# Performance work log

Hardware: AMD Instinct MI355X
Metric: run time of the kernel (lower is better)

## Reference

```python
import jax, jax.numpy as jnp
import numpy as np
from jax import lax

TAU = 10.0
THR = 1.0
ALPHA = float(np.exp(-1.0 / TAU))  # leak factor exp(-dt/tau), dt=1


def conv2d(x, w, pad):
    # x: [N,C,H,W], w: [O,I,kh,kw]
    return lax.conv_general_dilated(
        x, w, window_strides=(1, 1), padding=[(pad, pad), (pad, pad)],
        dimension_numbers=('NCHW', 'OIHW', 'NCHW'))


def avgpool(x, k):
    n, c, h, w = x.shape
    return x.reshape(n, c, h // k, k, w // k, k).mean(axis=(3, 5))


def exp_leak(x):
    # x: [T, ...]; v[t] = alpha*v[t-1] + x[t]; outputs membrane each step
    def step(v, xt):
        v = ALPHA * v + xt
        return v, v
    _, y = lax.scan(step, jnp.zeros_like(x[0]), x)
    return y


def lif(x):
    # LIF with SingleSpike + MembraneSubtract reset (norm_input=False)
    def step(v, xt):
        v = ALPHA * v + xt
        s = (v >= THR).astype(v.dtype)
        return v - s * THR, s
    _, s = lax.scan(step, jnp.zeros_like(x[0]), x)
    return s


def forward(x, conv1_w, conv2_w, lin_w):
    B, T = x.shape[:2]
    h = avgpool(conv2d(x.reshape(B * T, 2, 32, 32), conv1_w, 2), 4)  # [BT,4,8,8]
    h = h.reshape(B, T, 4, 8, 8).swapaxes(0, 1)                       # [T,B,4,8,8]
    h = lif(exp_leak(h)).swapaxes(0, 1).reshape(B * T, 4, 8, 8)
    h = avgpool(conv2d(h, conv2_w, 1), 2)                             # [BT,8,4,4]
    h = h.reshape(B, T, 8, 4, 4).swapaxes(0, 1)                       # [T,B,8,4,4]
    h = lif(exp_leak(h)).swapaxes(0, 1).reshape(B, T, 8 * 4 * 4)      # [B,T,128]
    return jnp.einsum('btf,of->bto', h, lin_w)                        # [B,T,2]


def setup_inputs() -> dict:
    key = jax.random.key(0)
    k1, k2, k3, k4 = jax.random.split(key, 4)
    B, T = 128, 100
    x = jax.random.uniform(k1, (B, T, 2, 32, 32), dtype=jnp.float32)
    conv1_w = jax.random.normal(k2, (4, 2, 5, 5), dtype=jnp.float32) / np.sqrt(2 * 5 * 5)
    conv2_w = jax.random.normal(k3, (8, 4, 3, 3), dtype=jnp.float32) / np.sqrt(4 * 3 * 3)
    lin_w = jax.random.normal(k4, (2, 128), dtype=jnp.float32) / np.sqrt(128)
    return {'x': x, 'conv1_w': conv1_w, 'conv2_w': conv2_w, 'lin_w': lin_w}


def reference(x, conv1_w, conv2_w, lin_w):
    return forward(x, conv1_w, conv2_w, lin_w)
```

## Files before the change

kernel.cpp:

```cpp
#include <hip/hip_runtime.h>

#define ALPHA 0.90483741803595957f

__global__ void prep_weights(const float* __restrict__ w1, const float* __restrict__ w2,
                             float* __restrict__ w1e, float* __restrict__ w2e) {
    int idx = blockIdx.x * 256 + threadIdx.x;
    if (idx < 512) {
        int v = idx & 7, u = (idx >> 3) & 7, ch = (idx >> 6) & 1, oc = idx >> 7;
        float s = 0.f;
        for (int a = 0; a < 5; ++a) {
            int i = u - a; if (i < 0 || i > 3) continue;
            for (int b = 0; b < 5; ++b) {
                int j = v - b; if (j < 0 || j > 3) continue;
                s += w1[((oc * 2 + ch) * 5 + a) * 5 + b];
            }
        }
        w1e[idx] = s * (1.f / 16.f);
    } else if (idx < 1024) {
        int k = idx - 512;
        int v = k & 3, u = (k >> 2) & 3, ch = (k >> 4) & 3, oc = k >> 6;
        float s = 0.f;
        for (int a = 0; a < 3; ++a) {
            int i = u - a; if (i < 0 || i > 1) continue;
            for (int b = 0; b < 3; ++b) {
                int j = v - b; if (j < 0 || j > 1) continue;
                s += w2[((oc * 4 + ch) * 3 + a) * 3 + b];
            }
        }
        w2e[k] = s * 0.25f;
    }
}

__global__ __launch_bounds__(256) void conv1_pool(const float* __restrict__ x,
                                                  const float* __restrict__ w1e,
                                                  float* __restrict__ y1) {
    __shared__ __align__(16) float tile[4][2][36][40];
    __shared__ __align__(16) float wlds[512];
    int tid = threadIdx.x;

    float4* t4 = (float4*)&tile[0][0][0][0];
    #pragma unroll
    for (int k = 0; k < 12; ++k) {
        int i = tid + k * 256;
        if (i < 2880) t4[i] = make_float4(0.f, 0.f, 0.f, 0.f);
    }
    for (int j = tid; j < 512; j += 256) {
        int oc = j >> 7, ch = (j >> 6) & 1, r = (j >> 3) & 7, c = j & 7;
        wlds[((ch * 8 + r) * 4 + oc) * 8 + c] = w1e[j];
    }
    __syncthreads();

    int w = tid >> 6, lane = tid & 63;
    long gi = (long)blockIdx.x * 4 + w;
    const float* src = x + gi * 2048;
    #pragma unroll
    for (int k = 0; k < 8; ++k) {
        int e = k * 256 + lane * 4;
        float4 d = *(const float4*)(src + e);
        int ch = e >> 10, rem = e & 1023, r = rem >> 5, c = rem & 31;
        float* dst = &tile[w][ch][r + 2][c + 2];
        *(float2*)dst = make_float2(d.x, d.y);
        *(float2*)(dst + 2) = make_float2(d.z, d.w);
    }

    int p = lane >> 3, q = lane & 7;
    float acc0 = 0.f, acc1 = 0.f, acc2 = 0.f, acc3 = 0.f;
    #pragma unroll
    for (int ch = 0; ch < 2; ++ch) {
        #pragma unroll
        for (int r = 0; r < 8; ++r) {
            const float* row = &tile[w][ch][4 * p + r][4 * q];
            float4 a = *(const float4*)row;
            float4 b = *(const float4*)(row + 4);
            const float* wr = &wlds[(ch * 8 + r) * 32];
            float4 wa, wb;
            wa = *(const float4*)(wr + 0);  wb = *(const float4*)(wr + 4);
            acc0 += wa.x * a.x + wa.y * a.y + wa.z * a.z + wa.w * a.w
                  + wb.x * b.x + wb.y * b.y + wb.z * b.z + wb.w * b.w;
            wa = *(const float4*)(wr + 8);  wb = *(const float4*)(wr + 12);
            acc1 += wa.x * a.x + wa.y * a.y + wa.z * a.z + wa.w * a.w
                  + wb.x * b.x + wb.y * b.y + wb.z * b.z + wb.w * b.w;
            wa = *(const float4*)(wr + 16); wb = *(const float4*)(wr + 20);
            acc2 += wa.x * a.x + wa.y * a.y + wa.z * a.z + wa.w * a.w
                  + wb.x * b.x + wb.y * b.y + wb.z * b.z + wb.w * b.w;
            wa = *(const float4*)(wr + 24); wb = *(const float4*)(wr + 28);
            acc3 += wa.x * a.x + wa.y * a.y + wa.z * a.z + wa.w * a.w
                  + wb.x * b.x + wb.y * b.y + wb.z * b.z + wb.w * b.w;
        }
    }
    float* dst = y1 + gi * 256 + lane;
    dst[0] = acc0; dst[64] = acc1; dst[128] = acc2; dst[192] = acc3;
}

__global__ __launch_bounds__(128, 1) void fused_rest(const float* __restrict__ y1,
                                                     const float* __restrict__ w2e,
                                                     const float* __restrict__ lw,
                                                     float* __restrict__ out) {
    __shared__ __align__(16) float spk[4][10][12];
    __shared__ __align__(16) float s2all[100][132];
    __shared__ __align__(16) float lwl[256];
    int tid = threadIdx.x;
    int b = blockIdx.x;

    for (int i = tid; i < 480; i += 128) ((float*)spk)[i] = 0.f;
    ((float2*)lwl)[tid] = ((const float2*)lw)[tid];

    int oc = tid >> 4, p = (tid >> 2) & 3, q = tid & 3;
    const float4* wp = (const float4*)(w2e + oc * 64);
    float4 w00 = wp[0],  w01 = wp[1],  w02 = wp[2],  w03 = wp[3];
    float4 w04 = wp[4],  w05 = wp[5],  w06 = wp[6],  w07 = wp[7];
    float4 w08 = wp[8],  w09 = wp[9],  w10 = wp[10], w11 = wp[11];
    float4 w12 = wp[12], w13 = wp[13], w14 = wp[14], w15 = wp[15];

    int ch1 = tid >> 6, r1 = (tid >> 3) & 7, c1 = tid & 7;
    const float* yp = y1 + (long)b * 25600 + tid;
    float v1a0 = 0.f, v1b0 = 0.f, v1a1 = 0.f, v1b1 = 0.f;
    float v2a = 0.f, v2b = 0.f;
    float xt0 = yp[0], xt1 = yp[128];
    __syncthreads();

#define C2(cc, rr, W, P) { const float* rowp = &spk[cc][2 * p + (rr)][2 * q];      \
        float2 a_ = *(const float2*)rowp; float2 b_ = *(const float2*)(rowp + 2);  \
        P += W.x * a_.x + W.y * a_.y + W.z * b_.x + W.w * b_.y; }

    for (int t = 0; t < 100; ++t) {
        float xn0 = 0.f, xn1 = 0.f;
        if (t < 99) {
            const float* ypn = yp + (t + 1) * 256;
            xn0 = ypn[0]; xn1 = ypn[128];
        }
        v1a0 = ALPHA * v1a0 + xt0; v1b0 = ALPHA * v1b0 + v1a0;
        float s0 = (v1b0 >= 1.f) ? 1.f : 0.f; v1b0 -= s0;
        spk[ch1][r1 + 1][c1 + 1] = s0;
        v1a1 = ALPHA * v1a1 + xt1; v1b1 = ALPHA * v1b1 + v1a1;
        float s1 = (v1b1 >= 1.f) ? 1.f : 0.f; v1b1 -= s1;
        spk[ch1 + 2][r1 + 1][c1 + 1] = s1;
        xt0 = xn0; xt1 = xn1;
        __syncthreads();

        float p0 = 0.f, p1 = 0.f, p2 = 0.f, p3 = 0.f;
        C2(0, 0, w00, p0) C2(0, 1, w01, p0) C2(0, 2, w02, p0) C2(0, 3, w03, p0)
        C2(1, 0, w04, p1) C2(1, 1, w05, p1) C2(1, 2, w06, p1) C2(1, 3, w07, p1)
        C2(2, 0, w08, p2) C2(2, 1, w09, p2) C2(2, 2, w10, p2) C2(2, 3, w11, p2)
        C2(3, 0, w12, p3) C2(3, 1, w13, p3) C2(3, 2, w14, p3) C2(3, 3, w15, p3)
        float acc = (p0 + p1) + (p2 + p3);

        v2a = ALPHA * v2a + acc; v2b = ALPHA * v2b + v2a;
        float ss = (v2b >= 1.f) ? 1.f : 0.f; v2b -= ss;
        s2all[t][tid] = ss;
        __syncthreads();
    }
#undef C2

    if (tid < 100) {
        const float4* sa  = (const float4*)&s2all[tid][0];
        const float4* lw4 = (const float4*)lwl;
        float e0a = 0.f, e0b = 0.f, e1a = 0.f, e1b = 0.f;
        #pragma unroll
        for (int k = 0; k < 32; k += 2) {
            float4 A = sa[k], B = sa[k + 1];
            float4 u0 = lw4[k], u1 = lw4[k + 1];
            float4 v0 = lw4[32 + k], v1 = lw4[33 + k];
            e0a += A.x * u0.x + A.y * u0.y + A.z * u0.z + A.w * u0.w;
            e0b += B.x * u1.x + B.y * u1.y + B.z * u1.z + B.w * u1.w;
            e1a += A.x * v0.x + A.y * v0.y + A.z * v0.z + A.w * v0.w;
            e1b += B.x * v1.x + B.y * v1.y + B.z * v1.z + B.w * v1.w;
        }
        float2 res = make_float2(e0a + e0b, e1a + e1b);
        *(float2*)(out + (long)b * 200 + tid * 2) = res;
    }
}

extern "C" void kernel_launch(void* const* d_in, const int* in_sizes, int n_in,
                              void* d_out, int out_size, void* d_ws, size_t ws_size,
                              hipStream_t stream) {
    const float* x  = (const float*)d_in[0];
    const float* w1 = (const float*)d_in[1];
    const float* w2 = (const float*)d_in[2];
    const float* lw = (const float*)d_in[3];
    float* out = (float*)d_out;

    float* ws  = (float*)d_ws;
    float* w1e = ws;
    float* w2e = ws + 512;
    float* y1  = ws + 1024;

    prep_weights<<<4, 256, 0, stream>>>(w1, w2, w1e, w2e);
    conv1_pool<<<3200, 256, 0, stream>>>(x, w1e, y1);
    fused_rest<<<128, 128, 0, stream>>>(y1, w2e, lw, out);
}
```

Measured before the change: 218.1 us.

## Split fused recurrent kernel into scan1, scan2 and linear kernels via global memory

Replaces the single 128-block fused kernel, which ran both LIF scans, conv2 and the linear layer with two barriers per timestep, with separate kernels. scan1 runs the first LIF per feature and writes padded spike maps to global memory. scan2 runs conv2 plus the second LIF across 256 single-wave blocks with no barriers. A shuffle-reduction kernel then does the linear layer. conv1_pool now assigns two images per block, each wave producing two output channels for half the work. The aim is to remove per-step __syncthreads latency and spread the serial scans over more blocks, at the cost of roughly 25MB of extra global spike traffic, a zeroing kernel, and more launches.

```diff
diff --git a/kernel.cpp b/kernel.cpp
--- a/kernel.cpp
+++ b/kernel.cpp
@@ -31,18 +31,22 @@
     }
 }
 
+__global__ __launch_bounds__(256) void zero_spk(float4* __restrict__ p) {
+    p[blockIdx.x * 256 + threadIdx.x] = make_float4(0.f, 0.f, 0.f, 0.f);
+}
+
 __global__ __launch_bounds__(256) void conv1_pool(const float* __restrict__ x,
                                                   const float* __restrict__ w1e,
                                                   float* __restrict__ y1) {
-    __shared__ __align__(16) float tile[4][2][36][40];
+    __shared__ __align__(16) float tile[2][2][36][40];
     __shared__ __align__(16) float wlds[512];
     int tid = threadIdx.x;
 
     float4* t4 = (float4*)&tile[0][0][0][0];
     #pragma unroll
-    for (int k = 0; k < 12; ++k) {
+    for (int k = 0; k < 6; ++k) {
         int i = tid + k * 256;
-        if (i < 2880) t4[i] = make_float4(0.f, 0.f, 0.f, 0.f);
+        if (i < 1440) t4[i] = make_float4(0.f, 0.f, 0.f, 0.f);
     }
     for (int j = tid; j < 512; j += 256) {
         int oc = j >> 7, ch = (j >> 6) & 1, r = (j >> 3) & 7, c = j & 7;
@@ -51,124 +55,124 @@
     __syncthreads();
 
     int w = tid >> 6, lane = tid & 63;
-    long gi = (long)blockIdx.x * 4 + w;
-    const float* src = x + gi * 2048;
-    #pragma unroll
-    for (int k = 0; k < 8; ++k) {
+    int im = w >> 1, half = w & 1;
+    long gi = (long)blockIdx.x * 2 + im;
+    const float* src = x + gi * 2048 + half * 1024;
+    #pragma unroll
+    for (int k = 0; k < 4; ++k) {
         int e = k * 256 + lane * 4;
         float4 d = *(const float4*)(src + e);
-        int ch = e >> 10, rem = e & 1023, r = rem >> 5, c = rem & 31;
-        float* dst = &tile[w][ch][r + 2][c + 2];
+        int r = e >> 5, c = e & 31;
+        float* dst = &tile[im][half][r + 2][c + 2];
         *(float2*)dst = make_float2(d.x, d.y);
         *(float2*)(dst + 2) = make_float2(d.z, d.w);
     }
-
+    __syncthreads();
+
+    int ocp = w & 1;
     int p = lane >> 3, q = lane & 7;
-    float acc0 = 0.f, acc1 = 0.f, acc2 = 0.f, acc3 = 0.f;
+    float acc0 = 0.f, acc1 = 0.f;
     #pragma unroll
     for (int ch = 0; ch < 2; ++ch) {
         #pragma unroll
         for (int r = 0; r < 8; ++r) {
-            const float* row = &tile[w][ch][4 * p + r][4 * q];
+            const float* row = &tile[im][ch][4 * p + r][4 * q];
             float4 a = *(const float4*)row;
             float4 b = *(const float4*)(row + 4);
-            const float* wr = &wlds[(ch * 8 + r) * 32];
-            float4 wa, wb;
-            wa = *(const float4*)(wr + 0);  wb = *(const float4*)(wr + 4);
+            const float* wr = &wlds[((ch * 8 + r) * 4 + ocp * 2) * 8];
+            float4 wa = *(const float4*)(wr + 0), wb = *(const float4*)(wr + 4);
             acc0 += wa.x * a.x + wa.y * a.y + wa.z * a.z + wa.w * a.w
                   + wb.x * b.x + wb.y * b.y + wb.z * b.z + wb.w * b.w;
-            wa = *(const float4*)(wr + 8);  wb = *(const float4*)(wr + 12);
+            wa = *(const float4*)(wr + 8); wb = *(const float4*)(wr + 12);
             acc1 += wa.x * a.x + wa.y * a.y + wa.z * a.z + wa.w * a.w
                   + wb.x * b.x + wb.y * b.y + wb.z * b.z + wb.w * b.w;
-            wa = *(const float4*)(wr + 16); wb = *(const float4*)(wr + 20);
-            acc2 += wa.x * a.x + wa.y * a.y + wa.z * a.z + wa.w * a.w
-                  + wb.x * b.x + wb.y * b.y + wb.z * b.z + wb.w * b.w;
-            wa = *(const float4*)(wr + 24); wb = *(const float4*)(wr + 28);
-            acc3 += wa.x * a.x + wa.y * a.y + wa.z * a.z + wa.w * a.w
-                  + wb.x * b.x + wb.y * b.y + wb.z * b.z + wb.w * b.w;
-        }
-    }
-    float* dst = y1 + gi * 256 + lane;
-    dst[0] = acc0; dst[64] = acc1; dst[128] = acc2; dst[192] = acc3;
-}
-
-__global__ __launch_bounds__(128, 1) void fused_rest(const float* __restrict__ y1,
-                                                     const float* __restrict__ w2e,
-                                                     const float* __restrict__ lw,
-                                                     float* __restrict__ out) {
-    __shared__ __align__(16) float spk[4][10][12];
-    __shared__ __align__(16) float s2all[100][132];
-    __shared__ __align__(16) float lwl[256];
-    int tid = threadIdx.x;
-    int b = blockIdx.x;
-
-    for (int i = tid; i < 480; i += 128) ((float*)spk)[i] = 0.f;
-    ((float2*)lwl)[tid] = ((const float2*)lw)[tid];
-
-    int oc = tid >> 4, p = (tid >> 2) & 3, q = tid & 3;
+        }
+    }
+    float* dst = y1 + gi * 256 + ocp * 128 + lane;
+    dst[0] = acc0; dst[64] = acc1;
+}
+
+__global__ __launch_bounds__(256) void scan1(const float* __restrict__ y1,
+                                             float* __restrict__ spk) {
+    int idx = blockIdx.x * 256 + threadIdx.x;
+    int b = idx >> 8, f = idx & 255;
+    int ch = f >> 6, r = (f >> 3) & 7, c = f & 7;
+    const float* p = y1 + (long)b * 25600 + f;
+    float* o = spk + (long)b * 48000 + ch * 120 + (r + 1) * 12 + (c + 1);
+    float v1 = 0.f, v2 = 0.f;
+    float c0 = p[0], c1 = p[256], c2 = p[512], c3 = p[768];
+    for (int t = 0; t < 100; t += 4) {
+        float n0 = 0.f, n1 = 0.f, n2 = 0.f, n3 = 0.f;
+        if (t < 96) {
+            const float* pp = p + (t + 4) * 256;
+            n0 = pp[0]; n1 = pp[256]; n2 = pp[512]; n3 = pp[768];
+        }
+        v1 = ALPHA * v1 + c0; v2 = ALPHA * v2 + v1;
+        float s = (v2 >= 1.f) ? 1.f : 0.f; v2 -= s; o[t * 480] = s;
+        v1 = ALPHA * v1 + c1; v2 = ALPHA * v2 + v1;
+        s = (v2 >= 1.f) ? 1.f : 0.f; v2 -= s; o[(t + 1) * 480] = s;
+        v1 = ALPHA * v1 + c2; v2 = ALPHA * v2 + v1;
+        s = (v2 >= 1.f) ? 1.f : 0.f; v2 -= s; o[(t + 2) * 480] = s;
+        v1 = ALPHA * v1 + c3; v2 = ALPHA * v2 + v1;
+        s = (v2 >= 1.f) ? 1.f : 0.f; v2 -= s; o[(t + 3) * 480] = s;
+        c0 = n0; c1 = n1; c2 = n2; c3 = n3;
+    }
+}
+
+__global__ __launch_bounds__(64, 1) void scan2(const float* __restrict__ spk,
+                                               const float* __restrict__ w2e,
+                                               float* __restrict__ s2) {
+    int b = blockIdx.x >> 1, h = blockIdx.x & 1;
+    int g = h * 64 + threadIdx.x;
+    int oc = g >> 4, p = (g >> 2) & 3, q = g & 3;
+
     const float4* wp = (const float4*)(w2e + oc * 64);
     float4 w00 = wp[0],  w01 = wp[1],  w02 = wp[2],  w03 = wp[3];
     float4 w04 = wp[4],  w05 = wp[5],  w06 = wp[6],  w07 = wp[7];
     float4 w08 = wp[8],  w09 = wp[9],  w10 = wp[10], w11 = wp[11];
     float4 w12 = wp[12], w13 = wp[13], w14 = wp[14], w15 = wp[15];
 
-    int ch1 = tid >> 6, r1 = (tid >> 3) & 7, c1 = tid & 7;
-    const float* yp = y1 + (long)b * 25600 + tid;
-    float v1a0 = 0.f, v1b0 = 0.f, v1a1 = 0.f, v1b1 = 0.f;
+    const float* sp = spk + (long)b * 48000;
+    float* os = s2 + (long)b * 12800 + g;
     float v2a = 0.f, v2b = 0.f;
-    float xt0 = yp[0], xt1 = yp[128];
-    __syncthreads();
-
-#define C2(cc, rr, W, P) { const float* rowp = &spk[cc][2 * p + (rr)][2 * q];      \
-        float2 a_ = *(const float2*)rowp; float2 b_ = *(const float2*)(rowp + 2);  \
+
+#define C2(cc, rr, W, P) { const float* rowp = st + (cc) * 120 + (2 * p + (rr)) * 12 + 2 * q; \
+        float2 a_ = *(const float2*)rowp; float2 b_ = *(const float2*)(rowp + 2);             \
         P += W.x * a_.x + W.y * a_.y + W.z * b_.x + W.w * b_.y; }
 
+    #pragma unroll 2
     for (int t = 0; t < 100; ++t) {
-        float xn0 = 0.f, xn1 = 0.f;
-        if (t < 99) {
-            const float* ypn = yp + (t + 1) * 256;
-            xn0 = ypn[0]; xn1 = ypn[128];
-        }
-        v1a0 = ALPHA * v1a0 + xt0; v1b0 = ALPHA * v1b0 + v1a0;
-        float s0 = (v1b0 >= 1.f) ? 1.f : 0.f; v1b0 -= s0;
-        spk[ch1][r1 + 1][c1 + 1] = s0;
-        v1a1 = ALPHA * v1a1 + xt1; v1b1 = ALPHA * v1b1 + v1a1;
-        float s1 = (v1b1 >= 1.f) ? 1.f : 0.f; v1b1 -= s1;
-        spk[ch1 + 2][r1 + 1][c1 + 1] = s1;
-        xt0 = xn0; xt1 = xn1;
-        __syncthreads();
-
+        const float* st = sp + t * 480;
         float p0 = 0.f, p1 = 0.f, p2 = 0.f, p3 = 0.f;
         C2(0, 0, w00, p0) C2(0, 1, w01, p0) C2(0, 2, w02, p0) C2(0, 3, w03, p0)
         C2(1, 0, w04, p1) C2(1, 1, w05, p1) C2(1, 2, w06, p1) C2(1, 3, w07, p1)
         C2(2, 0, w08, p2) C2(2, 1, w09, p2) C2(2, 2, w10, p2) C2(2, 3, w11, p2)
         C2(3, 0, w12, p3) C2(3, 1, w13, p3) C2(3, 2, w14, p3) C2(3, 3, w15, p3)
         float acc = (p0 + p1) + (p2 + p3);
-
         v2a = ALPHA * v2a + acc; v2b = ALPHA * v2b + v2a;
         float ss = (v2b >= 1.f) ? 1.f : 0.f; v2b -= ss;
-        s2all[t][tid] = ss;
-        __syncthreads();
+        os[t * 128] = ss;
     }
 #undef C2
-
-    if (tid < 100) {
-        const float4* sa  = (const float4*)&s2all[tid][0];
-        const float4* lw4 = (const float4*)lwl;
-        float e0a = 0.f, e0b = 0.f, e1a = 0.f, e1b = 0.f;
-        #pragma unroll
-        for (int k = 0; k < 32; k += 2) {
-            float4 A = sa[k], B = sa[k + 1];
-            float4 u0 = lw4[k], u1 = lw4[k + 1];
-            float4 v0 = lw4[32 + k], v1 = lw4[33 + k];
-            e0a += A.x * u0.x + A.y * u0.y + A.z * u0.z + A.w * u0.w;
-            e0b += B.x * u1.x + B.y * u1.y + B.z * u1.z + B.w * u1.w;
-            e1a += A.x * v0.x + A.y * v0.y + A.z * v0.z + A.w * v0.w;
-            e1b += B.x * v1.x + B.y * v1.y + B.z * v1.z + B.w * v1.w;
-        }
-        float2 res = make_float2(e0a + e0b, e1a + e1b);
-        *(float2*)(out + (long)b * 200 + tid * 2) = res;
-    }
+}
+
+__global__ __launch_bounds__(256) void linear_out(const float* __restrict__ s2,
+                                                  const float* __restrict__ lw,
+                                                  float* __restrict__ out) {
+    int tid = threadIdx.x;
+    long bt = (long)blockIdx.x * 4 + (tid >> 6);
+    int lane = tid & 63;
+    float2 v = *(const float2*)(s2 + bt * 128 + lane * 2);
+    float w00 = lw[lane * 2], w01 = lw[lane * 2 + 1];
+    float w10 = lw[128 + lane * 2], w11 = lw[128 + lane * 2 + 1];
+    float a0 = v.x * w00 + v.y * w01;
+    float a1 = v.x * w10 + v.y * w11;
+    #pragma unroll
+    for (int off = 32; off; off >>= 1) {
+        a0 += __shfl_down(a0, off);
+        a1 += __shfl_down(a1, off);
+    }
+    if (lane == 0) { out[bt * 2] = a0; out[bt * 2 + 1] = a1; }
 }
 
 extern "C" void kernel_launch(void* const* d_in, const int* in_sizes, int n_in,
@@ -184,8 +188,13 @@
     float* w1e = ws;
     float* w2e = ws + 512;
     float* y1  = ws + 1024;
+    float* spk = y1 + 3276800;
+    float* s2  = spk + 6144000;
 
     prep_weights<<<4, 256, 0, stream>>>(w1, w2, w1e, w2e);
-    conv1_pool<<<3200, 256, 0, stream>>>(x, w1e, y1);
-    fused_rest<<<128, 128, 0, stream>>>(y1, w2e, lw, out);
-}
+    zero_spk<<<6000, 256, 0, stream>>>((float4*)spk);
+    conv1_pool<<<6400, 256, 0, stream>>>(x, w1e, y1);
+    scan1<<<128, 256, 0, stream>>>(y1, spk);
+    scan2<<<256, 64, 0, stream>>>(spk, w2e, s2);
+    linear_out<<<3200, 256, 0, stream>>>(s2, lw, out);
+}
```

After: 321.9 us. 47.6% more time.
